# Kernel tuning notes

Measured on AMD Instinct MI355X. Metric: run time of the kernel, lower is better.

The kernel has to match this reference:

```python
import jax, jax.numpy as jnp
import numpy as np
import math

D_MODEL = 1024
N_HEADS = 16
HEAD_DIM = D_MODEL // N_HEADS
BAND_RADIUS = 2
BAND_VAL = 0.1


def setup_inputs() -> dict:
    key = jax.random.key(0)
    ks = jax.random.split(key, 12)
    B, S = 4, 2048
    scale = 1.0 / math.sqrt(D_MODEL)
    inp = {
        "x": jax.random.normal(ks[0], (B, S, D_MODEL), dtype=jnp.float32),
        "ocr_context": jax.random.normal(ks[1], (B, S, D_MODEL), dtype=jnp.float32),
        "Wq": jax.random.normal(ks[2], (D_MODEL, D_MODEL), dtype=jnp.float32) * scale,
        "bq": jnp.zeros((D_MODEL,), dtype=jnp.float32),
        "Wk": jax.random.normal(ks[3], (D_MODEL, D_MODEL), dtype=jnp.float32) * scale,
        "bk": jnp.zeros((D_MODEL,), dtype=jnp.float32),
        "Wv": jax.random.normal(ks[4], (D_MODEL, D_MODEL), dtype=jnp.float32) * scale,
        "bv": jnp.zeros((D_MODEL,), dtype=jnp.float32),
        "Wo": jax.random.normal(ks[5], (D_MODEL, D_MODEL), dtype=jnp.float32) * scale,
        "bo": jnp.zeros((D_MODEL,), dtype=jnp.float32),
        "ocr_bias": jax.random.normal(ks[6], (D_MODEL,), dtype=jnp.float32),
    }
    return inp


def _band_mask(S, dtype):
    # additive mask: 0.1 inside |i-j| <= 2, else 0 (matches _create_ocr_pattern_mask)
    i = jnp.arange(S)
    band = (jnp.abs(i[:, None] - i[None, :]) <= BAND_RADIUS).astype(dtype) * BAND_VAL
    return band[None, None, :, :]  # [1,1,S,S], broadcasts over batch & heads


def reference(x, ocr_context, Wq, bq, Wk, bk, Wv, bv, Wo, bo, ocr_bias):
    B, S, _ = x.shape
    # torch Linear: x @ W.T + b
    q = x @ Wq.T + bq + ocr_bias  # ocr bias added to q before head split
    k = x @ Wk.T + bk
    v = x @ Wv.T + bv
    q = q.reshape(B, S, N_HEADS, HEAD_DIM).transpose(0, 2, 1, 3)  # [B,H,S,d]
    k = k.reshape(B, S, N_HEADS, HEAD_DIM).transpose(0, 2, 1, 3)
    v = v.reshape(B, S, N_HEADS, HEAD_DIM).transpose(0, 2, 1, 3)
    scores = jnp.einsum("bhsd,bhtd->bhst", q, k) / math.sqrt(HEAD_DIM)
    scores = scores + _band_mask(S, scores.dtype)  # ocr_context only supplies shape
    attn = jax.nn.softmax(scores, axis=-1)
    out = jnp.einsum("bhst,bhtd->bhsd", attn, v)
    out = out.transpose(0, 2, 1, 3).reshape(B, S, D_MODEL)
    return out @ Wo.T + bo
```

## Files before the change

kernel.cpp:

```cpp
#include <hip/hip_runtime.h>
#include <hip/hip_bf16.h>
#include <stdint.h>

typedef __attribute__((ext_vector_type(8))) short bf16x8;
typedef __attribute__((ext_vector_type(4))) short bf16x4;
typedef __attribute__((ext_vector_type(4))) float f32x4;

#define L2E 1.4426950408889634f

static __device__ __forceinline__ unsigned short f2bf(float f) {
    __hip_bfloat16 h = __float2bfloat16(f);
    return __builtin_bit_cast(unsigned short, h);
}

static __device__ __forceinline__ void gl2lds16(const void* g, void* l) {
    __builtin_amdgcn_global_load_lds(
        (const __attribute__((address_space(1))) void*)g,
        (__attribute__((address_space(3))) void*)l,
        16, 0, 0);
}

__global__ void cast_kernel(const float* __restrict__ src,
                            unsigned short* __restrict__ dst, int n4) {
    int i = blockIdx.x * blockDim.x + threadIdx.x;
    int stride = gridDim.x * blockDim.x;
    for (; i < n4; i += stride) {
        float4 v = ((const float4*)src)[i];
        ushort4 o;
        o.x = f2bf(v.x); o.y = f2bf(v.y); o.z = f2bf(v.z); o.w = f2bf(v.w);
        ((ushort4*)dst)[i] = o;
    }
}

template<int OM>
__global__ __launch_bounds__(256) void gemm_bt(
    const unsigned short* __restrict__ A,
    const unsigned short* __restrict__ W,
    const float* __restrict__ bias,
    const float* __restrict__ bias2,
    float scale,
    unsigned short* __restrict__ obf,
    float* __restrict__ of)
{
    constexpr int K = 1024;
    __shared__ unsigned short As[128][64];
    __shared__ unsigned short Bs[128][64];

    const int tid  = threadIdx.x;
    const int wave = tid >> 6, lane = tid & 63;
    const int li = lane & 15, lg = lane >> 4;
    const int m0 = blockIdx.y * 128, n0 = blockIdx.x * 128;
    const int wm = (wave >> 1) * 64, wn = (wave & 1) * 64;

    const int srow = wave * 8 + (lane >> 3);
    const int scol = (lane & 7) * 8;

    f32x4 acc[4][4] = {};

    for (int k0 = 0; k0 < K; k0 += 64) {
#pragma unroll
        for (int rnd = 0; rnd < 4; ++rnd)
            gl2lds16(A + (size_t)(m0 + rnd * 32 + srow) * K + k0 + scol,
                     &As[rnd * 32 + wave * 8][0]);
#pragma unroll
        for (int rnd = 0; rnd < 4; ++rnd)
            gl2lds16(W + (size_t)(n0 + rnd * 32 + srow) * K + k0 + scol,
                     &Bs[rnd * 32 + wave * 8][0]);
        __syncthreads();
#pragma unroll
        for (int kk = 0; kk < 64; kk += 32) {
            bf16x8 af[4], bfr[4];
#pragma unroll
            for (int m = 0; m < 4; ++m)
                af[m] = *(const bf16x8*)&As[wm + m * 16 + li][kk + lg * 8];
#pragma unroll
            for (int n = 0; n < 4; ++n)
                bfr[n] = *(const bf16x8*)&Bs[wn + n * 16 + li][kk + lg * 8];
#pragma unroll
            for (int m = 0; m < 4; ++m)
#pragma unroll
                for (int n = 0; n < 4; ++n)
                    acc[m][n] = __builtin_amdgcn_mfma_f32_16x16x32_bf16(
                        af[m], bfr[n], acc[m][n], 0, 0, 0);
        }
        __syncthreads();
    }

#pragma unroll
    for (int n = 0; n < 4; ++n) {
        const int col = n0 + wn + n * 16 + li;
        float bb = bias[col];
        if (bias2) bb += bias2[col];
#pragma unroll
        for (int m = 0; m < 4; ++m) {
            if (OM == 2) {
                const int row0 = m0 + wm + m * 16 + lg * 4;
                size_t addr = ((size_t)(((row0 >> 11) << 4) + (col >> 6)) * 64 + (col & 63)) * 2048
                              + (row0 & 2047);
                ushort4 o;
                o.x = f2bf((acc[m][n][0] + bb) * scale);
                o.y = f2bf((acc[m][n][1] + bb) * scale);
                o.z = f2bf((acc[m][n][2] + bb) * scale);
                o.w = f2bf((acc[m][n][3] + bb) * scale);
                *(ushort4*)&obf[addr] = o;
            } else {
#pragma unroll
                for (int r = 0; r < 4; ++r) {
                    const int row = m0 + wm + m * 16 + lg * 4 + r;
                    float v = (acc[m][n][r] + bb) * scale;
                    if (OM == 1) of[(size_t)row * 1024 + col] = v;
                    else         obf[(size_t)row * 1024 + col] = f2bf(v);
                }
            }
        }
    }
}

__global__ __launch_bounds__(256, 3) void attn_kernel(
    const unsigned short* __restrict__ Q,
    const unsigned short* __restrict__ Km,
    const unsigned short* __restrict__ VT,
    unsigned short* __restrict__ AO)
{
    __shared__ unsigned short Ks[2][4096];
    __shared__ unsigned short Vs[2][4096];
    __shared__ unsigned short Ps[2][4][1024];

    const int tid  = threadIdx.x;
    const int w = tid >> 6, lane = tid & 63;
    const int li = lane & 15, lg = lane >> 4, li7 = li & 7;

    const int p  = blockIdx.y * 16 + blockIdx.x;
    const int q_ = (p & 7) * 128 + (p >> 3);
    const int bx = q_ & 15, bh = q_ >> 4;
    const int b = bh >> 4, h = bh & 15;
    const int q0 = bx * 128;
    const int qb0 = q0 + w * 32;

    const int srow = w * 16 + (lane >> 3);
    const int swz  = ((lane & 7) ^ (lane >> 3)) * 8;

    const unsigned short* Kg0 = Km + (size_t)(b * 2048 + srow) * 1024 + h * 64 + swz;
    const unsigned short* Vg0 = VT + ((size_t)bh * 64 + srow) * 2048 + swz;

    bf16x8 qf[2][2];
#pragma unroll
    for (int s = 0; s < 2; ++s)
#pragma unroll
        for (int t = 0; t < 2; ++t)
            qf[s][t] = *(const bf16x8*)&Q[(size_t)(b * 2048 + qb0 + s * 16 + li) * 1024
                                          + h * 64 + t * 32 + lg * 8];

    f32x4 acc[2][4] = {};
    float lr[2] = {0.f, 0.f};

#pragma unroll
    for (int it = 0; it < 2; ++it) {
        gl2lds16(Kg0 + (size_t)(it * 8) * 1024, &Ks[0][(w * 2 + it) * 512]);
        gl2lds16(Vg0 + (size_t)(it * 8) * 2048, &Vs[0][(w * 2 + it) * 512]);
    }
    __syncthreads();

    for (int t = 0; t < 32; ++t) {
        const int buf = t & 1;
        const int j0 = t * 64;
        if (t < 31) {
            const int j1 = j0 + 64;
#pragma unroll
            for (int it = 0; it < 2; ++it) {
                gl2lds16(Kg0 + (size_t)(j1 + it * 8) * 1024, &Ks[buf ^ 1][(w * 2 + it) * 512]);
                gl2lds16(Vg0 + (size_t)(it * 8) * 2048 + j1, &Vs[buf ^ 1][(w * 2 + it) * 512]);
            }
        }

        bf16x8 kf[2][4];
#pragma unroll
        for (int tt = 0; tt < 2; ++tt)
#pragma unroll
            for (int jf = 0; jf < 4; ++jf)
                kf[tt][jf] = *(const bf16x8*)&Ks[buf][(jf * 16 + li) * 64
                                                      + ((tt * 4 + lg) ^ li7) * 8];

#pragma unroll
        for (int s = 0; s < 2; ++s) {
            f32x4 st[4];
#pragma unroll
            for (int jf = 0; jf < 4; ++jf) {
                f32x4 z = {};
                z = __builtin_amdgcn_mfma_f32_16x16x32_bf16(kf[0][jf], qf[s][0], z, 0, 0, 0);
                st[jf] = __builtin_amdgcn_mfma_f32_16x16x32_bf16(kf[1][jf], qf[s][1], z, 0, 0, 0);
            }
            const int qb = qb0 + s * 16;
            if (j0 + 65 >= qb && j0 <= qb + 17) {
#pragma unroll
                for (int jf = 0; jf < 4; ++jf)
#pragma unroll
                    for (int r = 0; r < 4; ++r) {
                        int dq = (qb + li) - (j0 + jf * 16 + lg * 4 + r);
                        if ((unsigned)(dq + 2) <= 4u) st[jf][r] += 0.1f * L2E;
                    }
            }
            float ps = 0.f;
#pragma unroll
            for (int jf = 0; jf < 4; ++jf) {
                float p0 = __builtin_amdgcn_exp2f(st[jf][0]);
                float p1 = __builtin_amdgcn_exp2f(st[jf][1]);
                float p2 = __builtin_amdgcn_exp2f(st[jf][2]);
                float p3 = __builtin_amdgcn_exp2f(st[jf][3]);
                ps += (p0 + p1) + (p2 + p3);
                bf16x4 pk;
                pk[0] = (short)f2bf(p0); pk[1] = (short)f2bf(p1);
                pk[2] = (short)f2bf(p2); pk[3] = (short)f2bf(p3);
                *(bf16x4*)&Ps[s][w][li * 64 + ((jf * 2 + (lg >> 1)) ^ li7) * 8
                                    + (lg & 1) * 4] = pk;
            }
            lr[s] += ps;
        }

        bf16x8 vf[2][4];
#pragma unroll
        for (int tt = 0; tt < 2; ++tt)
#pragma unroll
            for (int db = 0; db < 4; ++db)
                vf[tt][db] = *(const bf16x8*)&Vs[buf][(db * 16 + li) * 64
                                                      + ((tt * 4 + lg) ^ li7) * 8];
#pragma unroll
        for (int s = 0; s < 2; ++s) {
            bf16x8 pf0 = *(const bf16x8*)&Ps[s][w][li * 64 + ((0 + lg) ^ li7) * 8];
            bf16x8 pf1 = *(const bf16x8*)&Ps[s][w][li * 64 + ((4 + lg) ^ li7) * 8];
#pragma unroll
            for (int db = 0; db < 4; ++db) {
                acc[s][db] = __builtin_amdgcn_mfma_f32_16x16x32_bf16(vf[0][db], pf0, acc[s][db], 0, 0, 0);
                acc[s][db] = __builtin_amdgcn_mfma_f32_16x16x32_bf16(vf[1][db], pf1, acc[s][db], 0, 0, 0);
            }
        }
        __syncthreads();
    }

#pragma unroll
    for (int s = 0; s < 2; ++s) {
        float l2 = lr[s] + __shfl_xor(lr[s], 16);
        l2 += __shfl_xor(l2, 32);
        const float inv = 1.f / l2;
#pragma unroll
        for (int db = 0; db < 4; ++db) {
            ushort4 o;
            o.x = f2bf(acc[s][db][0] * inv); o.y = f2bf(acc[s][db][1] * inv);
            o.z = f2bf(acc[s][db][2] * inv); o.w = f2bf(acc[s][db][3] * inv);
            *(ushort4*)&AO[(size_t)(b * 2048 + qb0 + s * 16 + li) * 1024
                           + h * 64 + db * 16 + lg * 4] = o;
        }
    }
}

extern "C" void kernel_launch(void* const* d_in, const int* in_sizes, int n_in,
                              void* d_out, int out_size, void* d_ws, size_t ws_size,
                              hipStream_t stream) {
    const float* x   = (const float*)d_in[0];
    const float* Wq  = (const float*)d_in[2];
    const float* bq  = (const float*)d_in[3];
    const float* Wk  = (const float*)d_in[4];
    const float* bk  = (const float*)d_in[5];
    const float* Wv  = (const float*)d_in[6];
    const float* bv  = (const float*)d_in[7];
    const float* Wo  = (const float*)d_in[8];
    const float* bo  = (const float*)d_in[9];
    const float* ocr = (const float*)d_in[10];
    float* out = (float*)d_out;

    char* ws = (char*)d_ws;
    const size_t MB = 1024 * 1024;
    unsigned short* xb  = (unsigned short*)(ws);
    unsigned short* Wqb = (unsigned short*)(ws + 16 * MB);
    unsigned short* Wkb = (unsigned short*)(ws + 18 * MB);
    unsigned short* Wvb = (unsigned short*)(ws + 20 * MB);
    unsigned short* Wob = (unsigned short*)(ws + 22 * MB);
    unsigned short* Qb  = (unsigned short*)(ws + 24 * MB);
    unsigned short* Kb  = (unsigned short*)(ws + 40 * MB);
    unsigned short* VTb = (unsigned short*)(ws + 56 * MB);
    unsigned short* AO  = xb;

    cast_kernel<<<2048, 256, 0, stream>>>(x,  xb,  8388608 / 4);
    cast_kernel<<<512,  256, 0, stream>>>(Wq, Wqb, 1048576 / 4);
    cast_kernel<<<512,  256, 0, stream>>>(Wk, Wkb, 1048576 / 4);
    cast_kernel<<<512,  256, 0, stream>>>(Wv, Wvb, 1048576 / 4);
    cast_kernel<<<512,  256, 0, stream>>>(Wo, Wob, 1048576 / 4);

    dim3 g(8, 64);
    const float QSC = 0.125f * L2E;
    gemm_bt<0><<<g, 256, 0, stream>>>(xb, Wqb, bq, ocr,     QSC, Qb,  nullptr);
    gemm_bt<0><<<g, 256, 0, stream>>>(xb, Wkb, bk, nullptr, 1.f, Kb,  nullptr);
    gemm_bt<2><<<g, 256, 0, stream>>>(xb, Wvb, bv, nullptr, 1.f, VTb, nullptr);

    attn_kernel<<<dim3(16, 64), 256, 0, stream>>>(Qb, Kb, VTb, AO);

    gemm_bt<1><<<g, 256, 0, stream>>>(AO, Wob, bo, nullptr, 1.f, nullptr, out);
}
```

Measured before the change: 229.5 us.

## Keep softmax probabilities in registers via lane permutes instead of LDS round-trip

Removes the shared-memory P buffer. The bf16 probabilities are packed into registers and rearranged into MFMA B-operand layout with v_permlane32_swap and ds_swizzle. This cuts LDS writes and reads plus LDS footprint, which allows raising occupancy via launch_bounds 4. It also wraps the MFMA phases in s_setprio so waves doing matrix math get issue priority over the others. The permute logic is intricate and may add register pressure.

```diff
diff --git a/kernel.cpp b/kernel.cpp
--- a/kernel.cpp
+++ b/kernel.cpp
@@ -5,6 +5,7 @@
 typedef __attribute__((ext_vector_type(8))) short bf16x8;
 typedef __attribute__((ext_vector_type(4))) short bf16x4;
 typedef __attribute__((ext_vector_type(4))) float f32x4;
+typedef __attribute__((ext_vector_type(4))) unsigned u32x4;
 
 #define L2E 1.4426950408889634f
 
@@ -116,7 +117,7 @@
     }
 }
 
-__global__ __launch_bounds__(256, 3) void attn_kernel(
+__global__ __launch_bounds__(256, 4) void attn_kernel(
     const unsigned short* __restrict__ Q,
     const unsigned short* __restrict__ Km,
     const unsigned short* __restrict__ VT,
@@ -124,7 +125,6 @@
 {
     __shared__ unsigned short Ks[2][4096];
     __shared__ unsigned short Vs[2][4096];
-    __shared__ unsigned short Ps[2][4][1024];
 
     const int tid  = threadIdx.x;
     const int w = tid >> 6, lane = tid & 63;
@@ -181,15 +181,18 @@
                 kf[tt][jf] = *(const bf16x8*)&Ks[buf][(jf * 16 + li) * 64
                                                       + ((tt * 4 + lg) ^ li7) * 8];
 
+        unsigned pw[2][8];
 #pragma unroll
         for (int s = 0; s < 2; ++s) {
             f32x4 st[4];
+            __builtin_amdgcn_s_setprio(1);
 #pragma unroll
             for (int jf = 0; jf < 4; ++jf) {
                 f32x4 z = {};
                 z = __builtin_amdgcn_mfma_f32_16x16x32_bf16(kf[0][jf], qf[s][0], z, 0, 0, 0);
                 st[jf] = __builtin_amdgcn_mfma_f32_16x16x32_bf16(kf[1][jf], qf[s][1], z, 0, 0, 0);
             }
+            __builtin_amdgcn_s_setprio(0);
             const int qb = qb0 + s * 16;
             if (j0 + 65 >= qb && j0 <= qb + 17) {
 #pragma unroll
@@ -208,13 +211,34 @@
                 float p2 = __builtin_amdgcn_exp2f(st[jf][2]);
                 float p3 = __builtin_amdgcn_exp2f(st[jf][3]);
                 ps += (p0 + p1) + (p2 + p3);
-                bf16x4 pk;
-                pk[0] = (short)f2bf(p0); pk[1] = (short)f2bf(p1);
-                pk[2] = (short)f2bf(p2); pk[3] = (short)f2bf(p3);
-                *(bf16x4*)&Ps[s][w][li * 64 + ((jf * 2 + (lg >> 1)) ^ li7) * 8
-                                    + (lg & 1) * 4] = pk;
+                pw[s][jf * 2 + 0] = (unsigned)f2bf(p0) | ((unsigned)f2bf(p1) << 16);
+                pw[s][jf * 2 + 1] = (unsigned)f2bf(p2) | ((unsigned)f2bf(p3) << 16);
             }
             lr[s] += ps;
+
+#pragma unroll
+            for (int c = 0; c < 2; ++c)
+#pragma unroll
+                for (int pp = 0; pp < 2; ++pp) {
+                    unsigned a0 = pw[s][c * 4 + pp];
+                    unsigned b0 = pw[s][c * 4 + 2 + pp];
+                    asm volatile("v_permlane32_swap_b32 %0, %1"
+                                 : "+v"(a0), "+v"(b0));
+                    pw[s][c * 4 + pp] = a0;
+                    pw[s][c * 4 + 2 + pp] = b0;
+                }
+            const bool bhi = (lane & 16) != 0;
+#pragma unroll
+            for (int c = 0; c < 2; ++c)
+#pragma unroll
+                for (int pp = 0; pp < 2; ++pp) {
+                    unsigned s0 = pw[s][c * 4 + pp];
+                    unsigned s1 = pw[s][c * 4 + 2 + pp];
+                    unsigned sel = bhi ? s0 : s1;
+                    unsigned got = (unsigned)__builtin_amdgcn_ds_swizzle((int)sel, 0x401F);
+                    pw[s][c * 4 + pp]     = bhi ? got : s0;
+                    pw[s][c * 4 + 2 + pp] = bhi ? s1 : got;
+                }
         }
 
         bf16x8 vf[2][4];
@@ -224,16 +248,20 @@
             for (int db = 0; db < 4; ++db)
                 vf[tt][db] = *(const bf16x8*)&Vs[buf][(db * 16 + li) * 64
                                                       + ((tt * 4 + lg) ^ li7) * 8];
+        __builtin_amdgcn_s_setprio(1);
 #pragma unroll
         for (int s = 0; s < 2; ++s) {
-            bf16x8 pf0 = *(const bf16x8*)&Ps[s][w][li * 64 + ((0 + lg) ^ li7) * 8];
-            bf16x8 pf1 = *(const bf16x8*)&Ps[s][w][li * 64 + ((4 + lg) ^ li7) * 8];
+            u32x4 t0 = {pw[s][0], pw[s][1], pw[s][2], pw[s][3]};
+            u32x4 t1 = {pw[s][4], pw[s][5], pw[s][6], pw[s][7]};
+            bf16x8 pf0 = __builtin_bit_cast(bf16x8, t0);
+            bf16x8 pf1 = __builtin_bit_cast(bf16x8, t1);
 #pragma unroll
             for (int db = 0; db < 4; ++db) {
                 acc[s][db] = __builtin_amdgcn_mfma_f32_16x16x32_bf16(vf[0][db], pf0, acc[s][db], 0, 0, 0);
                 acc[s][db] = __builtin_amdgcn_mfma_f32_16x16x32_bf16(vf[1][db], pf1, acc[s][db], 0, 0, 0);
             }
         }
+        __builtin_amdgcn_s_setprio(0);
         __syncthreads();
     }
 
```

Measured after the change: 251.8 us. 1.1x slower.

## Use 32x32 MFMA with in-register P transpose via permlane32_swap in attention

Applied to the files above, without the earlier changes.

Attention switches from 16x16x32 to 32x32x16 bf16 MFMA tiles. The P matrix is rearranged in registers with v_permlane32_swap instead of going through an LDS round trip, which removes the Ps shared buffer and its barrier traffic. s_setprio is added around the MFMA sections, occupancy in launch_bounds goes from 3 to 4, and the GEMM block order is swizzled for better L2 reuse. The risks are register pressure at 4 waves per SIMD and whether the permlane layout is correct.

```diff
diff --git a/kernel.cpp b/kernel.cpp
--- a/kernel.cpp
+++ b/kernel.cpp
@@ -3,8 +3,9 @@
 #include <stdint.h>
 
 typedef __attribute__((ext_vector_type(8))) short bf16x8;
-typedef __attribute__((ext_vector_type(4))) short bf16x4;
 typedef __attribute__((ext_vector_type(4))) float f32x4;
+typedef __attribute__((ext_vector_type(16))) float f32x16;
+typedef __attribute__((ext_vector_type(4))) unsigned u32x4;
 
 #define L2E 1.4426950408889634f
 
@@ -49,7 +50,9 @@
     const int tid  = threadIdx.x;
     const int wave = tid >> 6, lane = tid & 63;
     const int li = lane & 15, lg = lane >> 4;
-    const int m0 = blockIdx.y * 128, n0 = blockIdx.x * 128;
+    const int lin = blockIdx.y * 8 + blockIdx.x;
+    const int n2  = (lin & 7) * 64 + (lin >> 3);
+    const int m0 = (n2 >> 3) * 128, n0 = (n2 & 7) * 128;
     const int wm = (wave >> 1) * 64, wn = (wave & 1) * 64;
 
     const int srow = wave * 8 + (lane >> 3);
@@ -116,7 +119,7 @@
     }
 }
 
-__global__ __launch_bounds__(256, 3) void attn_kernel(
+__global__ __launch_bounds__(256, 4) void attn_kernel(
     const unsigned short* __restrict__ Q,
     const unsigned short* __restrict__ Km,
     const unsigned short* __restrict__ VT,
@@ -124,18 +127,17 @@
 {
     __shared__ unsigned short Ks[2][4096];
     __shared__ unsigned short Vs[2][4096];
-    __shared__ unsigned short Ps[2][4][1024];
 
     const int tid  = threadIdx.x;
     const int w = tid >> 6, lane = tid & 63;
-    const int li = lane & 15, lg = lane >> 4, li7 = li & 7;
+    const int li5 = lane & 31, l5 = lane >> 5, li7 = li5 & 7;
 
     const int p  = blockIdx.y * 16 + blockIdx.x;
     const int q_ = (p & 7) * 128 + (p >> 3);
     const int bx = q_ & 15, bh = q_ >> 4;
     const int b = bh >> 4, h = bh & 15;
-    const int q0 = bx * 128;
-    const int qb0 = q0 + w * 32;
+    const int qb = bx * 128 + w * 32;
+    const int qrow = qb + li5;
 
     const int srow = w * 16 + (lane >> 3);
     const int swz  = ((lane & 7) ^ (lane >> 3)) * 8;
@@ -143,16 +145,14 @@
     const unsigned short* Kg0 = Km + (size_t)(b * 2048 + srow) * 1024 + h * 64 + swz;
     const unsigned short* Vg0 = VT + ((size_t)bh * 64 + srow) * 2048 + swz;
 
-    bf16x8 qf[2][2];
-#pragma unroll
-    for (int s = 0; s < 2; ++s)
-#pragma unroll
-        for (int t = 0; t < 2; ++t)
-            qf[s][t] = *(const bf16x8*)&Q[(size_t)(b * 2048 + qb0 + s * 16 + li) * 1024
-                                          + h * 64 + t * 32 + lg * 8];
-
-    f32x4 acc[2][4] = {};
-    float lr[2] = {0.f, 0.f};
+    bf16x8 qf[4];
+#pragma unroll
+    for (int f = 0; f < 4; ++f)
+        qf[f] = *(const bf16x8*)&Q[(size_t)(b * 2048 + qrow) * 1024 + h * 64
+                                   + f * 16 + l5 * 8];
+
+    f32x16 acc[2] = {};
+    float lr = 0.f;
 
 #pragma unroll
     for (int it = 0; it < 2; ++it) {
@@ -173,84 +173,90 @@
             }
         }
 
-        bf16x8 kf[2][4];
-#pragma unroll
-        for (int tt = 0; tt < 2; ++tt)
-#pragma unroll
-            for (int jf = 0; jf < 4; ++jf)
-                kf[tt][jf] = *(const bf16x8*)&Ks[buf][(jf * 16 + li) * 64
-                                                      + ((tt * 4 + lg) ^ li7) * 8];
-
-#pragma unroll
-        for (int s = 0; s < 2; ++s) {
-            f32x4 st[4];
-#pragma unroll
-            for (int jf = 0; jf < 4; ++jf) {
-                f32x4 z = {};
-                z = __builtin_amdgcn_mfma_f32_16x16x32_bf16(kf[0][jf], qf[s][0], z, 0, 0, 0);
-                st[jf] = __builtin_amdgcn_mfma_f32_16x16x32_bf16(kf[1][jf], qf[s][1], z, 0, 0, 0);
-            }
-            const int qb = qb0 + s * 16;
-            if (j0 + 65 >= qb && j0 <= qb + 17) {
-#pragma unroll
-                for (int jf = 0; jf < 4; ++jf)
-#pragma unroll
-                    for (int r = 0; r < 4; ++r) {
-                        int dq = (qb + li) - (j0 + jf * 16 + lg * 4 + r);
-                        if ((unsigned)(dq + 2) <= 4u) st[jf][r] += 0.1f * L2E;
-                    }
-            }
-            float ps = 0.f;
-#pragma unroll
-            for (int jf = 0; jf < 4; ++jf) {
-                float p0 = __builtin_amdgcn_exp2f(st[jf][0]);
-                float p1 = __builtin_amdgcn_exp2f(st[jf][1]);
-                float p2 = __builtin_amdgcn_exp2f(st[jf][2]);
-                float p3 = __builtin_amdgcn_exp2f(st[jf][3]);
-                ps += (p0 + p1) + (p2 + p3);
-                bf16x4 pk;
-                pk[0] = (short)f2bf(p0); pk[1] = (short)f2bf(p1);
-                pk[2] = (short)f2bf(p2); pk[3] = (short)f2bf(p3);
-                *(bf16x4*)&Ps[s][w][li * 64 + ((jf * 2 + (lg >> 1)) ^ li7) * 8
-                                    + (lg & 1) * 4] = pk;
-            }
-            lr[s] += ps;
-        }
-
-        bf16x8 vf[2][4];
-#pragma unroll
-        for (int tt = 0; tt < 2; ++tt)
-#pragma unroll
-            for (int db = 0; db < 4; ++db)
-                vf[tt][db] = *(const bf16x8*)&Vs[buf][(db * 16 + li) * 64
-                                                      + ((tt * 4 + lg) ^ li7) * 8];
-#pragma unroll
-        for (int s = 0; s < 2; ++s) {
-            bf16x8 pf0 = *(const bf16x8*)&Ps[s][w][li * 64 + ((0 + lg) ^ li7) * 8];
-            bf16x8 pf1 = *(const bf16x8*)&Ps[s][w][li * 64 + ((4 + lg) ^ li7) * 8];
-#pragma unroll
-            for (int db = 0; db < 4; ++db) {
-                acc[s][db] = __builtin_amdgcn_mfma_f32_16x16x32_bf16(vf[0][db], pf0, acc[s][db], 0, 0, 0);
-                acc[s][db] = __builtin_amdgcn_mfma_f32_16x16x32_bf16(vf[1][db], pf1, acc[s][db], 0, 0, 0);
-            }
-        }
+        f32x16 st[2];
+        __builtin_amdgcn_s_setprio(1);
+#pragma unroll
+        for (int jf = 0; jf < 2; ++jf) {
+            f32x16 z = {};
+#pragma unroll
+            for (int f = 0; f < 4; ++f) {
+                bf16x8 kf = *(const bf16x8*)&Ks[buf][(jf * 32 + li5) * 64
+                                                     + ((f * 2 + l5) ^ li7) * 8];
+                z = __builtin_amdgcn_mfma_f32_32x32x16_bf16(kf, qf[f], z, 0, 0, 0);
+            }
+            st[jf] = z;
+        }
+        __builtin_amdgcn_s_setprio(0);
+
+        if (j0 >= qb - 65 && j0 <= qb + 33) {
+#pragma unroll
+            for (int jf = 0; jf < 2; ++jf)
+#pragma unroll
+                for (int r = 0; r < 16; ++r) {
+                    int j = j0 + jf * 32 + (r & 3) + 8 * (r >> 2) + 4 * l5;
+                    int dq = qrow - j;
+                    if ((unsigned)(dq + 2) <= 4u) st[jf][r] += 0.1f * L2E;
+                }
+        }
+
+        unsigned pw[2][8];
+        float ps = 0.f;
+#pragma unroll
+        for (int jf = 0; jf < 2; ++jf)
+#pragma unroll
+            for (int m = 0; m < 8; ++m) {
+                float p0 = __builtin_amdgcn_exp2f(st[jf][2 * m]);
+                float p1 = __builtin_amdgcn_exp2f(st[jf][2 * m + 1]);
+                ps += p0 + p1;
+                pw[jf][m] = (unsigned)f2bf(p0) | ((unsigned)f2bf(p1) << 16);
+            }
+        lr += ps;
+
+#pragma unroll
+        for (int jf = 0; jf < 2; ++jf)
+#pragma unroll
+            for (int m2 = 0; m2 < 2; ++m2)
+#pragma unroll
+                for (int m0_ = 0; m0_ < 2; ++m0_) {
+                    unsigned a0 = pw[jf][m2 * 4 + m0_];
+                    unsigned b0 = pw[jf][m2 * 4 + m0_ + 2];
+                    asm volatile("v_permlane32_swap_b32 %0, %1"
+                                 : "+v"(a0), "+v"(b0));
+                    pw[jf][m2 * 4 + m0_]     = a0;
+                    pw[jf][m2 * 4 + m0_ + 2] = b0;
+                }
+
+        __builtin_amdgcn_s_setprio(1);
+#pragma unroll
+        for (int db = 0; db < 2; ++db)
+#pragma unroll
+            for (int tt = 0; tt < 4; ++tt) {
+                bf16x8 vf = *(const bf16x8*)&Vs[buf][(db * 32 + li5) * 64
+                                                     + ((tt * 2 + l5) ^ li7) * 8];
+                const int jf = tt >> 1, m2 = tt & 1;
+                u32x4 tw = {pw[jf][m2 * 4 + 0], pw[jf][m2 * 4 + 1],
+                            pw[jf][m2 * 4 + 2], pw[jf][m2 * 4 + 3]};
+                acc[db] = __builtin_amdgcn_mfma_f32_32x32x16_bf16(
+                    vf, __builtin_bit_cast(bf16x8, tw), acc[db], 0, 0, 0);
+            }
+        __builtin_amdgcn_s_setprio(0);
         __syncthreads();
     }
 
-#pragma unroll
-    for (int s = 0; s < 2; ++s) {
-        float l2 = lr[s] + __shfl_xor(lr[s], 16);
-        l2 += __shfl_xor(l2, 32);
-        const float inv = 1.f / l2;
-#pragma unroll
-        for (int db = 0; db < 4; ++db) {
+    float l2 = lr + __shfl_xor(lr, 32);
+    const float inv = 1.f / l2;
+#pragma unroll
+    for (int db = 0; db < 2; ++db)
+#pragma unroll
+        for (int g = 0; g < 4; ++g) {
             ushort4 o;
-            o.x = f2bf(acc[s][db][0] * inv); o.y = f2bf(acc[s][db][1] * inv);
-            o.z = f2bf(acc[s][db][2] * inv); o.w = f2bf(acc[s][db][3] * inv);
-            *(ushort4*)&AO[(size_t)(b * 2048 + qb0 + s * 16 + li) * 1024
-                           + h * 64 + db * 16 + lg * 4] = o;
-        }
-    }
+            o.x = f2bf(acc[db][g * 4 + 0] * inv);
+            o.y = f2bf(acc[db][g * 4 + 1] * inv);
+            o.z = f2bf(acc[db][g * 4 + 2] * inv);
+            o.w = f2bf(acc[db][g * 4 + 3] * inv);
+            *(ushort4*)&AO[(size_t)(b * 2048 + qrow) * 1024 + h * 64
+                           + db * 32 + g * 8 + l5 * 4] = o;
+        }
 }
 
 extern "C" void kernel_launch(void* const* d_in, const int* in_sizes, int n_in,
```

New measurement: 229.8 us. About the same (+0.1%).
